# Kernel optimization log

Hardware: AMD Instinct MI355X
Metric: run time of the kernel (lower is better)

The kernel has to match this reference:

```python
import jax, jax.numpy as jnp
import numpy as np
from jax import lax

EPS = 1e-5  # torch BatchNorm2d default


def setup_inputs() -> dict:
    key = jax.random.key(0)
    k1, k2 = jax.random.split(key)
    x = jax.random.normal(k1, (8, 32, 28, 28), dtype=jnp.float32)
    # AdderConv.param: [out_channel, in_channel, k, k], init ~ N(0,1)
    W = jax.random.normal(k2, (64, 32, 3, 3), dtype=jnp.float32)
    # BatchNorm2d affine params at init
    gamma = jnp.ones((64,), dtype=jnp.float32)
    beta = jnp.zeros((64,), dtype=jnp.float32)
    return {"x": x, "W": W, "gamma": gamma, "beta": beta}


def _adder(patches, Wc):
    # patches: [N, K, Ho, Wo] with K = C*kh*kw (channel-major, matching torch unfold)
    # Wc: [O, K]
    # AdderNet: out[n,o,ho,wo] = -sum_k |patches[n,k,ho,wo] - Wc[o,k]|
    diff = patches[:, None, :, :, :] - Wc[None, :, :, None, None]  # [N,O,K,Ho,Wo]
    return -jnp.abs(diff).sum(axis=2)  # [N,O,Ho,Wo]


def reference(x, W, gamma, beta):
    O, C, kh, kw = W.shape
    # im2col, same layout as torch.nn.functional.unfold: feature dim = C*kh*kw
    patches = lax.conv_general_dilated_patches(
        x, (kh, kw), window_strides=(1, 1), padding=[(1, 1), (1, 1)]
    )  # [N, C*kh*kw, Ho, Wo]
    Wc = W.reshape(O, C * kh * kw)
    out = _adder(patches, Wc)  # [N, O, Ho, Wo]
    # BatchNorm2d, training mode (batch statistics, biased variance)
    mean = out.mean(axis=(0, 2, 3), keepdims=True)
    var = out.var(axis=(0, 2, 3), keepdims=True)
    y = (out - mean) * lax.rsqrt(var + EPS)
    return y * gamma[None, :, None, None] + beta[None, :, None, None]
```

## Files before the change

### kernel.cpp

```cpp
#include <hip/hip_runtime.h>

#define NB   8
#define CIN  32
#define HH   28
#define WW   28
#define OC   64
#define HWSZ (HH*WW)
#define TOTAL (NB*OC*HWSZ)
#define CNT  (NB*HWSZ)

#define TROWS 6
#define TCOLS 30
#define TSZ   (CIN*TROWS*TCOLS)

#define CPW   2
#define PHCC  8

__global__ __launch_bounds__(256) void adder_kernel(
    const float* __restrict__ x, const float* __restrict__ Wt,
    float* __restrict__ raw, double* __restrict__ stats)
{
    __shared__ float xs[TSZ];
    const int t     = threadIdx.x;
    const int bid   = blockIdx.x;
    const int chgrp = bid & 7;
    const int rq    = (bid >> 3) % 7;
    const int n     = bid / 56;
    const int h0    = rq * 4;

    for (int i = t; i < TSZ; i += 256) {
        int cc  = i / (TROWS*TCOLS);
        int rem = i % (TROWS*TCOLS);
        int r   = rem / TCOLS;
        int col = rem % TCOLS;
        int hh  = h0 - 1 + r;
        int ww  = col - 1;
        float v = 0.0f;
        if (hh >= 0 && hh < HH && ww >= 0 && ww < WW)
            v = x[((n*CIN + cc)*HH + hh)*WW + ww];
        xs[i] = v;
    }
    __syncthreads();

    const int lane = t & 63;
    const int g    = __builtin_amdgcn_readfirstlane(t >> 6);
    const int rg   = lane >> 5;
    const int pl   = lane & 31;
    const bool valid = pl < WW;
    const int pw   = valid ? pl : 0;
    const int o_base = chgrp*8 + g*CPW;

    float acc[2][CPW];
    #pragma unroll
    for (int pix = 0; pix < 2; ++pix)
        #pragma unroll
        for (int oo = 0; oo < CPW; ++oo) acc[pix][oo] = 0.0f;

    for (int ph = 0; ph < CIN/PHCC; ++ph) {
        const int cbase = ph * PHCC;

        float xr[PHCC][4][3];
        #pragma unroll
        for (int cc = 0; cc < PHCC; ++cc) {
            const int b0 = ((cbase+cc)*TROWS + 2*rg)*TCOLS + pw;
            #pragma unroll
            for (int dr = 0; dr < 4; ++dr)
                #pragma unroll
                for (int dc = 0; dc < 3; ++dc)
                    xr[cc][dr][dc] = xs[b0 + dr*TCOLS + dc];
        }

        #pragma unroll
        for (int oo = 0; oo < CPW; ++oo) {
            const float* wp = Wt + ((o_base + oo)*CIN + cbase)*9;
            #pragma unroll
            for (int cc = 0; cc < PHCC; ++cc) {
                #pragma unroll
                for (int dr = 0; dr < 3; ++dr)
                    #pragma unroll
                    for (int dc = 0; dc < 3; ++dc) {
                        float w = wp[cc*9 + dr*3 + dc];
                        acc[0][oo] += __builtin_fabsf(xr[cc][dr][dc]   - w);
                        acc[1][oo] += __builtin_fabsf(xr[cc][dr+1][dc] - w);
                    }
            }
        }
    }

    if (valid) {
        #pragma unroll
        for (int pix = 0; pix < 2; ++pix) {
            const int hh = h0 + 2*rg + pix;
            #pragma unroll
            for (int oo = 0; oo < CPW; ++oo)
                raw[((n*OC + o_base + oo)*HH + hh)*WW + pw] = -acc[pix][oo];
        }
    }

    #pragma unroll
    for (int oo = 0; oo < CPW; ++oo) {
        float v0 = valid ? -acc[0][oo] : 0.0f;
        float v1 = valid ? -acc[1][oo] : 0.0f;
        float s  = v0 + v1;
        float s2 = v0*v0 + v1*v1;
        #pragma unroll
        for (int off = 32; off >= 1; off >>= 1) {
            s  += __shfl_xor(s,  off, 64);
            s2 += __shfl_xor(s2, off, 64);
        }
        if (lane == 0) {
            atomicAdd(&stats[o_base + oo],      (double)s);
            atomicAdd(&stats[64 + o_base + oo], (double)s2);
        }
    }
}

__global__ __launch_bounds__(256) void bn_kernel(
    const float* __restrict__ raw, const double* __restrict__ stats,
    const float* __restrict__ gamma, const float* __restrict__ beta,
    float* __restrict__ out)
{
    int i4 = blockIdx.x * 256 + threadIdx.x;
    if (i4 >= TOTAL/4) return;
    int o = (i4 / (HWSZ/4)) & (OC - 1);
    double mean = stats[o] * (1.0 / CNT);
    double var  = stats[64 + o] * (1.0 / CNT) - mean * mean;
    double inv  = 1.0 / sqrt(var + 1e-5);
    double scl  = (double)gamma[o] * inv;
    float s = (float)scl;
    float b = (float)((double)beta[o] - mean * scl);
    float4 a = ((const float4*)raw)[i4];
    float4 v;
    v.x = a.x * s + b;
    v.y = a.y * s + b;
    v.z = a.z * s + b;
    v.w = a.w * s + b;
    ((float4*)out)[i4] = v;
}

extern "C" void kernel_launch(void* const* d_in, const int* in_sizes, int n_in,
                              void* d_out, int out_size, void* d_ws, size_t ws_size,
                              hipStream_t stream) {
    const float* x     = (const float*)d_in[0];
    const float* Wt    = (const float*)d_in[1];
    const float* gamma = (const float*)d_in[2];
    const float* beta  = (const float*)d_in[3];
    float* out = (float*)d_out;

    double* stats = (double*)d_ws;
    float*  raw   = (float*)((char*)d_ws + 4096);

    hipMemsetAsync(d_ws, 0, 1024, stream);

    adder_kernel<<<NB*7*8, 256, 0, stream>>>(x, Wt, raw, stats);
    bn_kernel<<<(TOTAL/4 + 255) / 256, 256, 0, stream>>>(raw, stats, gamma, beta, out);
}
```

Measured before the change: 93.23 us.

## Split input channels across waves and reduce partial sums through shared memory

Each of the four waves in a block now handles a quarter of the input channels for four output channels, and the partial sums are combined through shared memory before the write and the stats reduction. The grid doubles to 896 blocks, each covering 4 output channels instead of 8, and launch bounds request 3 blocks per SM. The goal is more parallelism and occupancy on the 256-CU part, with each wave's input tile loaded into registers only once. In exchange the input tile is staged to shared memory twice as often overall, and there is an extra block barrier plus a cross-wave reduction.

Result: slower. 95.71 us (+2.7%).

```diff
diff --git a/kernel.cpp b/kernel.cpp
--- a/kernel.cpp
+++ b/kernel.cpp
@@ -13,20 +13,22 @@
 #define TCOLS 30
 #define TSZ   (CIN*TROWS*TCOLS)
 
-#define CPW   2
-#define PHCC  8
+#define CPW   4
+#define QCC   8
 
-__global__ __launch_bounds__(256) void adder_kernel(
+__global__ __launch_bounds__(256, 3) void adder_kernel(
     const float* __restrict__ x, const float* __restrict__ Wt,
     float* __restrict__ raw, double* __restrict__ stats)
 {
     __shared__ float xs[TSZ];
-    const int t     = threadIdx.x;
-    const int bid   = blockIdx.x;
-    const int chgrp = bid & 7;
-    const int rq    = (bid >> 3) % 7;
-    const int n     = bid / 56;
-    const int h0    = rq * 4;
+    const int t   = threadIdx.x;
+    const int bid = blockIdx.x;
+    const int ocg = bid & 15;
+    const int tmp = bid >> 4;
+    const int rq  = tmp % 7;
+    const int n   = tmp / 7;
+    const int h0  = rq * 4;
+    const int o_base = ocg * CPW;
 
     for (int i = t; i < TSZ; i += 256) {
         int cc  = i / (TROWS*TCOLS);
@@ -48,7 +50,18 @@
     const int pl   = lane & 31;
     const bool valid = pl < WW;
     const int pw   = valid ? pl : 0;
-    const int o_base = chgrp*8 + g*CPW;
+    const int cbase = g * QCC;
+
+    float xr[QCC][4][3];
+    #pragma unroll
+    for (int cc = 0; cc < QCC; ++cc) {
+        const int b0 = ((cbase+cc)*TROWS + 2*rg)*TCOLS + pw;
+        #pragma unroll
+        for (int dr = 0; dr < 4; ++dr)
+            #pragma unroll
+            for (int dc = 0; dc < 3; ++dc)
+                xr[cc][dr][dc] = xs[b0 + dr*TCOLS + dc];
+    }
 
     float acc[2][CPW];
     #pragma unroll
@@ -56,61 +69,65 @@
         #pragma unroll
         for (int oo = 0; oo < CPW; ++oo) acc[pix][oo] = 0.0f;
 
-    for (int ph = 0; ph < CIN/PHCC; ++ph) {
-        const int cbase = ph * PHCC;
+    #pragma unroll
+    for (int oo = 0; oo < CPW; ++oo) {
+        const float* wp = Wt + ((o_base + oo)*CIN + cbase)*9;
+        #pragma unroll
+        for (int cc = 0; cc < QCC; ++cc) {
+            #pragma unroll
+            for (int dr = 0; dr < 3; ++dr)
+                #pragma unroll
+                for (int dc = 0; dc < 3; ++dc) {
+                    float w = wp[cc*9 + dr*3 + dc];
+                    acc[0][oo] += __builtin_fabsf(xr[cc][dr][dc]   - w);
+                    acc[1][oo] += __builtin_fabsf(xr[cc][dr+1][dc] - w);
+                }
+        }
+    }
 
-        float xr[PHCC][4][3];
+    __syncthreads();
+    float4* red = (float4*)xs;
+    if (g > 0) {
+        const int base = ((g-1)*64 + lane)*2;
+        red[base + 0] = *(float4*)&acc[0][0];
+        red[base + 1] = *(float4*)&acc[1][0];
+    }
+    __syncthreads();
+    if (g == 0) {
         #pragma unroll
-        for (int cc = 0; cc < PHCC; ++cc) {
-            const int b0 = ((cbase+cc)*TROWS + 2*rg)*TCOLS + pw;
+        for (int w = 0; w < 3; ++w) {
+            const int base = (w*64 + lane)*2;
+            float4 a0 = red[base + 0];
+            float4 a1 = red[base + 1];
+            acc[0][0] += a0.x; acc[0][1] += a0.y; acc[0][2] += a0.z; acc[0][3] += a0.w;
+            acc[1][0] += a1.x; acc[1][1] += a1.y; acc[1][2] += a1.z; acc[1][3] += a1.w;
+        }
+
+        if (valid) {
             #pragma unroll
-            for (int dr = 0; dr < 4; ++dr)
+            for (int pix = 0; pix < 2; ++pix) {
+                const int hh = h0 + 2*rg + pix;
                 #pragma unroll
-                for (int dc = 0; dc < 3; ++dc)
-                    xr[cc][dr][dc] = xs[b0 + dr*TCOLS + dc];
+                for (int oo = 0; oo < CPW; ++oo)
+                    raw[((n*OC + o_base + oo)*HH + hh)*WW + pw] = -acc[pix][oo];
+            }
         }
 
         #pragma unroll
         for (int oo = 0; oo < CPW; ++oo) {
-            const float* wp = Wt + ((o_base + oo)*CIN + cbase)*9;
+            float v0 = valid ? -acc[0][oo] : 0.0f;
+            float v1 = valid ? -acc[1][oo] : 0.0f;
+            float s  = v0 + v1;
+            float s2 = v0*v0 + v1*v1;
             #pragma unroll
-            for (int cc = 0; cc < PHCC; ++cc) {
-                #pragma unroll
-                for (int dr = 0; dr < 3; ++dr)
-                    #pragma unroll
-                    for (int dc = 0; dc < 3; ++dc) {
-                        float w = wp[cc*9 + dr*3 + dc];
-                        acc[0][oo] += __builtin_fabsf(xr[cc][dr][dc]   - w);
-                        acc[1][oo] += __builtin_fabsf(xr[cc][dr+1][dc] - w);
-                    }
+            for (int off = 32; off >= 1; off >>= 1) {
+                s  += __shfl_xor(s,  off, 64);
+                s2 += __shfl_xor(s2, off, 64);
             }
-        }
-    }
-
-    if (valid) {
-        #pragma unroll
-        for (int pix = 0; pix < 2; ++pix) {
-            const int hh = h0 + 2*rg + pix;
-            #pragma unroll
-            for (int oo = 0; oo < CPW; ++oo)
-                raw[((n*OC + o_base + oo)*HH + hh)*WW + pw] = -acc[pix][oo];
-        }
-    }
-
-    #pragma unroll
-    for (int oo = 0; oo < CPW; ++oo) {
-        float v0 = valid ? -acc[0][oo] : 0.0f;
-        float v1 = valid ? -acc[1][oo] : 0.0f;
-        float s  = v0 + v1;
-        float s2 = v0*v0 + v1*v1;
-        #pragma unroll
-        for (int off = 32; off >= 1; off >>= 1) {
-            s  += __shfl_xor(s,  off, 64);
-            s2 += __shfl_xor(s2, off, 64);
-        }
-        if (lane == 0) {
-            atomicAdd(&stats[o_base + oo],      (double)s);
-            atomicAdd(&stats[64 + o_base + oo], (double)s2);
+            if (lane == 0) {
+                atomicAdd(&stats[o_base + oo],      (double)s);
+                atomicAdd(&stats[64 + o_base + oo], (double)s2);
+            }
         }
     }
 }
@@ -152,6 +169,6 @@
 
     hipMemsetAsync(d_ws, 0, 1024, stream);
 
-    adder_kernel<<<NB*7*8, 256, 0, stream>>>(x, Wt, raw, stats);
+    adder_kernel<<<16*7*NB, 256, 0, stream>>>(x, Wt, raw, stats);
     bn_kernel<<<(TOTAL/4 + 255) / 256, 256, 0, stream>>>(raw, stats, gamma, beta, out);
 }
```
